# Optimization experiments

Measured on AMD Instinct MI355X. Metric: run time of the kernel, lower is better.

## Reference

```python
import jax, jax.numpy as jnp
import numpy as np

N_NODES = 100000
N_EDGES = 1600000
IN, HID, OUT = 128, 128, 64


def setup_inputs() -> dict:
    key = jax.random.key(0)
    ks = jax.random.split(key, 12)
    x = jax.random.normal(ks[0], (N_NODES, IN), dtype=jnp.float32)
    src = jax.random.randint(ks[1], (N_EDGES,), 0, N_NODES, dtype=jnp.int32)
    dst = jax.random.randint(ks[2], (N_EDGES,), 0, N_NODES, dtype=jnp.int32)

    def lin(k, fan_in, fan_out):
        return jax.random.normal(k, (fan_in, fan_out), dtype=jnp.float32) / jnp.sqrt(jnp.float32(fan_in))

    return {
        "x": x, "src": src, "dst": dst,
        "w_self_0": lin(ks[3], IN, HID), "w_neigh_0": lin(ks[4], IN, HID), "b_0": jnp.zeros((HID,), jnp.float32),
        "w_self_1": lin(ks[5], HID, HID), "w_neigh_1": lin(ks[6], HID, HID), "b_1": jnp.zeros((HID,), jnp.float32),
        "w_self_2": lin(ks[7], HID, OUT), "w_neigh_2": lin(ks[8], HID, OUT), "b_2": jnp.zeros((OUT,), jnp.float32),
    }


def reference(x, src, dst, w_self_0, w_neigh_0, b_0, w_self_1, w_neigh_1, b_1, w_self_2, w_neigh_2, b_2):
    n = x.shape[0]
    # in-degree per dst node; zero-degree nodes keep aggregated 0 (clamp avoids div-by-0)
    deg = jax.ops.segment_sum(jnp.ones_like(dst, dtype=x.dtype), dst, num_segments=n)
    inv_deg = (1.0 / jnp.maximum(deg, 1.0))[:, None]

    def sage_layer(h, w_s, w_n, b):
        # irregular gather of src features, segment-mean over dst
        agg = jax.ops.segment_sum(h[src], dst, num_segments=n) * inv_deg
        return h @ w_s + agg @ w_n + b

    h = jax.nn.relu(sage_layer(x, w_self_0, w_neigh_0, b_0))   # dropout = identity (eval)
    h = jax.nn.relu(sage_layer(h, w_self_1, w_neigh_1, b_1))
    return sage_layer(h, w_self_2, w_neigh_2, b_2)
```

## Files before the change

kernel.cpp:

```cpp
#include <hip/hip_runtime.h>


#define NN 100000
#define NE 1600000
#define BSH 7
#define BND 128
#define NB  782
#define NBLKS 512
#define EPB ((NE + NBLKS - 1) / NBLKS)
#define STOT (NB * NBLKS)
#define SCAN_E 2048
#define NSB ((STOT + SCAN_E - 1) / SCAN_E)
#define GEMM_BLOCKS 1563

typedef __attribute__((ext_vector_type(8))) short short8;
typedef __attribute__((ext_vector_type(4))) float f32x4;
typedef unsigned int uint;
typedef unsigned short ushort;

__device__ inline ushort f2bf(float f) {
    uint u = __float_as_uint(f);
    u += 0x7FFFu + ((u >> 16) & 1u);
    return (ushort)(u >> 16);
}
__device__ inline float bf_lo(uint w) { return __uint_as_float(w << 16); }
__device__ inline float bf_hi(uint w) { return __uint_as_float(w & 0xFFFF0000u); }

template<int NCS, int NCN, bool XF32, bool ABF, bool WLDS>
__device__ void gemm_body(int wid, int tid, int nthr,
    const void* __restrict__ Hv, const ushort* __restrict__ Wf,
    const float* __restrict__ bias, void* __restrict__ Av, ushort* __restrict__ Bt)
{
    constexpr int NCT = (NCS + NCN) / 16;
    const short8* wp;
    if constexpr (WLDS) {
        __shared__ short8 wl[NCT * 4 * 64];
        uint4* dl = (uint4*)wl;
        const uint4* sg = (const uint4*)Wf;
        for (int i = tid; i < NCT * 4 * 64; i += nthr) dl[i] = sg[i];
        __syncthreads();
        wp = wl;
    } else {
        wp = (const short8*)Wf;
    }
    if (wid >= NN / 16) return;
    const int lane = tid & 63;
    const int m = lane & 15;
    const int q = lane >> 4;

    short8 af[4];
    if (XF32) {
        const float* hp = (const float*)Hv + (size_t)(wid * 16 + m) * 128;
        #pragma unroll
        for (int kt = 0; kt < 4; ++kt) {
            const float4 f0 = *(const float4*)(hp + kt * 32 + q * 8);
            const float4 f1 = *(const float4*)(hp + kt * 32 + q * 8 + 4);
            short8 v;
            v[0] = (short)f2bf(f0.x); v[1] = (short)f2bf(f0.y);
            v[2] = (short)f2bf(f0.z); v[3] = (short)f2bf(f0.w);
            v[4] = (short)f2bf(f1.x); v[5] = (short)f2bf(f1.y);
            v[6] = (short)f2bf(f1.z); v[7] = (short)f2bf(f1.w);
            af[kt] = v;
        }
    } else {
        const short8* hp = (const short8*)((const ushort*)Hv + (size_t)(wid * 16 + m) * 128);
        #pragma unroll
        for (int kt = 0; kt < 4; ++kt) af[kt] = hp[kt * 4 + q];
    }

    f32x4 acc[NCT];
    #pragma unroll
    for (int i = 0; i < NCT; ++i) acc[i] = (f32x4){0.f, 0.f, 0.f, 0.f};

    #pragma unroll
    for (int ct = 0; ct < NCT; ++ct) {
        #pragma unroll
        for (int kt = 0; kt < 4; ++kt) {
            const short8 bf = wp[(ct * 4 + kt) * 64 + lane];
            acc[ct] = __builtin_amdgcn_mfma_f32_16x16x32_bf16(af[kt], bf, acc[ct], 0, 0, 0);
        }
    }

    const int r0 = wid * 16 + q * 4;
    #pragma unroll
    for (int ct = 0; ct < NCS / 16; ++ct) {
        const int c = ct * 16 + m;
        const float bv = bias[c];
        #pragma unroll
        for (int r = 0; r < 4; ++r) {
            const float v = acc[ct][r] + bv;
            if (ABF) ((ushort*)Av)[(size_t)(r0 + r) * NCS + c] = f2bf(v);
            else     ((float*) Av)[(size_t)(r0 + r) * NCS + c] = v;
        }
    }
    #pragma unroll
    for (int ct = NCS / 16; ct < NCT; ++ct) {
        const int c = ct * 16 + m - NCS;
        #pragma unroll
        for (int r = 0; r < 4; ++r)
            Bt[(size_t)(r0 + r) * NCN + c] = f2bf(acc[ct][r]);
    }
}

template<int NCS, int NCN, bool XF32, bool ABF>
__global__ __launch_bounds__(512) void gemm_mfma_k(
    const void* __restrict__ Hv, const ushort* __restrict__ Wf,
    const float* __restrict__ bias, void* __restrict__ Av, ushort* __restrict__ Bt)
{
    gemm_body<NCS, NCN, XF32, ABF, true>(
        (blockIdx.x * 512 + threadIdx.x) >> 6, threadIdx.x, 512, Hv, Wf, bias, Av, Bt);
}

__global__ __launch_bounds__(256) void phist_pack_k(
    const int* __restrict__ dst, int* __restrict__ histG,
    const float* __restrict__ ws0, const float* __restrict__ wn0, ushort* __restrict__ wf0,
    const float* __restrict__ ws1, const float* __restrict__ wn1, ushort* __restrict__ wf1,
    const float* __restrict__ ws2, const float* __restrict__ wn2, ushort* __restrict__ wf2)
{
    __shared__ int h[NB];
    const int t = threadIdx.x;
    if (blockIdx.x < NBLKS) {
        for (int i = t; i < NB; i += 256) h[i] = 0;
        __syncthreads();
        const int blk = blockIdx.x;
        const int e0 = blk * EPB;
        const int e1 = min(e0 + EPB, NE);
        for (int e = e0 + t; e < e1; e += 256)
            atomicAdd(&h[dst[e] >> BSH], 1);
        __syncthreads();
        for (int i = t; i < NB; i += 256)
            histG[i * NBLKS + blk] = h[i];
        return;
    }
    const int b = blockIdx.x - NBLKS;
    const float *ws, *wn; ushort* wf; int ncs, idx;
    if (b < 16)      { ws = ws0; wn = wn0; wf = wf0; ncs = 128; idx = b * 256 + t; }
    else if (b < 32) { ws = ws1; wn = wn1; wf = wf1; ncs = 128; idx = (b - 16) * 256 + t; }
    else             { ws = ws2; wn = wn2; wf = wf2; ncs = 64;  idx = (b - 32) * 256 + t; }
    const int total = (2 * ncs / 16) * 4 * 64;
    if (idx >= total) return;
    const int l = idx & 63;
    const int f = idx >> 6;
    const int kt = f & 3;
    const int ct = f >> 2;
    const int n = ct * 16 + (l & 15);
    const int k0 = kt * 32 + (l >> 4) * 8;
    uint w[4];
    #pragma unroll
    for (int p = 0; p < 4; ++p) {
        const int k = k0 + p * 2;
        float v0, v1;
        if (n < ncs) { v0 = ws[k * ncs + n];         v1 = ws[(k + 1) * ncs + n]; }
        else         { v0 = wn[k * ncs + (n - ncs)]; v1 = wn[(k + 1) * ncs + (n - ncs)]; }
        w[p] = (uint)f2bf(v0) | ((uint)f2bf(v1) << 16);
    }
    uint4 o; o.x = w[0]; o.y = w[1]; o.z = w[2]; o.w = w[3];
    ((uint4*)wf)[idx] = o;
}

__global__ __launch_bounds__(256) void scan1_k(int* __restrict__ data, int* __restrict__ blksum) {
    __shared__ int lds[256];
    const int t = threadIdx.x;
    const int base = blockIdx.x * SCAN_E + t * 8;
    int v[8];
    int s = 0;
    #pragma unroll
    for (int i = 0; i < 8; ++i) {
        const int idx = base + i;
        v[i] = (idx < STOT) ? data[idx] : 0;
        s += v[i];
    }
    lds[t] = s;
    __syncthreads();
    #pragma unroll
    for (int off = 1; off < 256; off <<= 1) {
        const int cur = lds[t];
        const int y = (t >= off) ? lds[t - off] : 0;
        __syncthreads();
        lds[t] = cur + y;
        __syncthreads();
    }
    const int incl = lds[t];
    if (t == 255) blksum[blockIdx.x] = incl;
    int run = incl - s;
    #pragma unroll
    for (int i = 0; i < 8; ++i) {
        const int idx = base + i;
        if (idx < STOT) data[idx] = run;
        run += v[i];
    }
}

__global__ __launch_bounds__(256) void scan3_k(int* __restrict__ data, const int* __restrict__ blksum) {
    __shared__ int lds[256];
    const int t = threadIdx.x;
    lds[t] = (t < NSB) ? blksum[t] : 0;
    __syncthreads();
    #pragma unroll
    for (int off = 1; off < 256; off <<= 1) {
        const int cur = lds[t];
        const int y = (t >= off) ? lds[t - off] : 0;
        __syncthreads();
        lds[t] = cur + y;
        __syncthreads();
    }
    const int add = (blockIdx.x == 0) ? 0 : lds[blockIdx.x - 1];
    const int base = blockIdx.x * SCAN_E + t * 8;
    #pragma unroll
    for (int i = 0; i < 8; ++i) {
        const int idx = base + i;
        if (idx < STOT) data[idx] += add;
    }
}

__global__ __launch_bounds__(256) void pscatter_gemm0_k(
    const int* __restrict__ src, const int* __restrict__ dst,
    const int* __restrict__ histG, int* __restrict__ pb,
    const float* __restrict__ x, const ushort* __restrict__ wf0,
    const float* __restrict__ b0, ushort* __restrict__ Abf, ushort* __restrict__ Bt)
{
    __shared__ int wc[NB];
    const int t = threadIdx.x;
    if (blockIdx.x < NBLKS) {
        const int blk = blockIdx.x;
        for (int i = t; i < NB; i += 256) wc[i] = histG[i * NBLKS + blk];
        __syncthreads();
        const int e0 = blk * EPB;
        const int e1 = min(e0 + EPB, NE);
        for (int e = e0 + t; e < e1; e += 256) {
            const int d = dst[e];
            const int pos = atomicAdd(&wc[d >> BSH], 1);
            pb[pos] = (src[e] << BSH) | (d & (BND - 1));
        }
        return;
    }
    gemm_body<128, 128, true, true, false>(
        ((blockIdx.x - NBLKS) * 256 + t) >> 6, t, 256, x, wf0, b0, Abf, Bt);
}

__global__ __launch_bounds__(256) void bucket_place_k(const int* __restrict__ histG,
                                                      const int* __restrict__ pb,
                                                      int* __restrict__ row,
                                                      int* __restrict__ esrc) {
    __shared__ int cnt[BND], wc[BND], excl[BND], scan[BND];
    const int b = blockIdx.x;
    const int t = threadIdx.x;
    if (t < BND) { cnt[t] = 0; wc[t] = 0; }
    __syncthreads();
    const int s0 = histG[b * NBLKS];
    const int s1 = (b + 1 < NB) ? histG[(b + 1) * NBLKS] : NE;
    for (int e = s0 + t; e < s1; e += 256)
        atomicAdd(&cnt[pb[e] & (BND - 1)], 1);
    __syncthreads();
    if (t < BND) scan[t] = cnt[t];
    __syncthreads();
    for (int off = 1; off < BND; off <<= 1) {
        int nv = 0;
        if (t < BND) {
            nv = scan[t];
            if (t >= off) nv += scan[t - off];
        }
        __syncthreads();
        if (t < BND) scan[t] = nv;
        __syncthreads();
    }
    if (t < BND) {
        const int ex = scan[t] - cnt[t];
        excl[t] = ex;
        const int node = b * BND + t;
        if (node <= NN) row[node] = s0 + ex;
    }
    __syncthreads();
    for (int e = s0 + t; e < s1; e += 256) {
        const int p = pb[e];
        const int dl = p & (BND - 1);
        const int pos = s0 + excl[dl] + atomicAdd(&wc[dl], 1);
        esrc[pos] = p >> BSH;
    }
}

__global__ __launch_bounds__(256) void agg128_k(
    const int* __restrict__ row, const int* __restrict__ esrc,
    const ushort* __restrict__ Bt, const ushort* __restrict__ Abf, ushort* __restrict__ Hb)
{
    const int node = (blockIdx.x * 256 + threadIdx.x) >> 4;
    const int ln = threadIdx.x & 15;
    if (node >= NN) return;
    const int e0 = row[node];
    const int e1 = row[node + 1];
    const uint4* B = (const uint4*)Bt;
    float a0 = 0.f, a1 = 0.f, a2 = 0.f, a3 = 0.f;
    float a4 = 0.f, a5 = 0.f, a6 = 0.f, a7 = 0.f;
    int e = e0;
    for (; e + 8 <= e1; e += 8) {
        int s[8];
        #pragma unroll
        for (int j = 0; j < 8; ++j) s[j] = esrc[e + j];
        uint4 v[8];
        #pragma unroll
        for (int j = 0; j < 8; ++j) v[j] = B[(size_t)s[j] * 16 + ln];
        #pragma unroll
        for (int j = 0; j < 8; ++j) {
            a0 += bf_lo(v[j].x); a1 += bf_hi(v[j].x);
            a2 += bf_lo(v[j].y); a3 += bf_hi(v[j].y);
            a4 += bf_lo(v[j].z); a5 += bf_hi(v[j].z);
            a6 += bf_lo(v[j].w); a7 += bf_hi(v[j].w);
        }
    }
    if (e + 4 <= e1) {
        int s[4];
        #pragma unroll
        for (int j = 0; j < 4; ++j) s[j] = esrc[e + j];
        uint4 v[4];
        #pragma unroll
        for (int j = 0; j < 4; ++j) v[j] = B[(size_t)s[j] * 16 + ln];
        #pragma unroll
        for (int j = 0; j < 4; ++j) {
            a0 += bf_lo(v[j].x); a1 += bf_hi(v[j].x);
            a2 += bf_lo(v[j].y); a3 += bf_hi(v[j].y);
            a4 += bf_lo(v[j].z); a5 += bf_hi(v[j].z);
            a6 += bf_lo(v[j].w); a7 += bf_hi(v[j].w);
        }
        e += 4;
    }
    for (; e < e1; ++e) {
        const uint4 v = B[(size_t)esrc[e] * 16 + ln];
        a0 += bf_lo(v.x); a1 += bf_hi(v.x);
        a2 += bf_lo(v.y); a3 += bf_hi(v.y);
        a4 += bf_lo(v.z); a5 += bf_hi(v.z);
        a6 += bf_lo(v.w); a7 += bf_hi(v.w);
    }
    const int deg = e1 - e0;
    const float invd = (deg > 0) ? 1.0f / (float)deg : 0.0f;
    const uint4 aw = ((const uint4*)Abf)[(size_t)node * 16 + ln];
    const float v0 = fmaxf(bf_lo(aw.x) + a0 * invd, 0.f);
    const float v1 = fmaxf(bf_hi(aw.x) + a1 * invd, 0.f);
    const float v2 = fmaxf(bf_lo(aw.y) + a2 * invd, 0.f);
    const float v3 = fmaxf(bf_hi(aw.y) + a3 * invd, 0.f);
    const float v4 = fmaxf(bf_lo(aw.z) + a4 * invd, 0.f);
    const float v5 = fmaxf(bf_hi(aw.z) + a5 * invd, 0.f);
    const float v6 = fmaxf(bf_lo(aw.w) + a6 * invd, 0.f);
    const float v7 = fmaxf(bf_hi(aw.w) + a7 * invd, 0.f);
    uint4 o;
    o.x = (uint)f2bf(v0) | ((uint)f2bf(v1) << 16);
    o.y = (uint)f2bf(v2) | ((uint)f2bf(v3) << 16);
    o.z = (uint)f2bf(v4) | ((uint)f2bf(v5) << 16);
    o.w = (uint)f2bf(v6) | ((uint)f2bf(v7) << 16);
    ((uint4*)Hb)[(size_t)node * 16 + ln] = o;
}

__global__ __launch_bounds__(256) void agg64_k(
    const int* __restrict__ row, const int* __restrict__ esrc,
    const ushort* __restrict__ Bt, float* __restrict__ out)
{
    const int node = (blockIdx.x * 256 + threadIdx.x) >> 3;
    const int ln = threadIdx.x & 7;
    if (node >= NN) return;
    const int e0 = row[node];
    const int e1 = row[node + 1];
    const uint4* B = (const uint4*)Bt;
    float a0 = 0.f, a1 = 0.f, a2 = 0.f, a3 = 0.f;
    float a4 = 0.f, a5 = 0.f, a6 = 0.f, a7 = 0.f;
    int e = e0;
    for (; e + 8 <= e1; e += 8) {
        int s[8];
        #pragma unroll
        for (int j = 0; j < 8; ++j) s[j] = esrc[e + j];
        uint4 v[8];
        #pragma unroll
        for (int j = 0; j < 8; ++j) v[j] = B[(size_t)s[j] * 8 + ln];
        #pragma unroll
        for (int j = 0; j < 8; ++j) {
            a0 += bf_lo(v[j].x); a1 += bf_hi(v[j].x);
            a2 += bf_lo(v[j].y); a3 += bf_hi(v[j].y);
            a4 += bf_lo(v[j].z); a5 += bf_hi(v[j].z);
            a6 += bf_lo(v[j].w); a7 += bf_hi(v[j].w);
        }
    }
    if (e + 4 <= e1) {
        int s[4];
        #pragma unroll
        for (int j = 0; j < 4; ++j) s[j] = esrc[e + j];
        uint4 v[4];
        #pragma unroll
        for (int j = 0; j < 4; ++j) v[j] = B[(size_t)s[j] * 8 + ln];
        #pragma unroll
        for (int j = 0; j < 4; ++j) {
            a0 += bf_lo(v[j].x); a1 += bf_hi(v[j].x);
            a2 += bf_lo(v[j].y); a3 += bf_hi(v[j].y);
            a4 += bf_lo(v[j].z); a5 += bf_hi(v[j].z);
            a6 += bf_lo(v[j].w); a7 += bf_hi(v[j].w);
        }
        e += 4;
    }
    for (; e < e1; ++e) {
        const uint4 v = B[(size_t)esrc[e] * 8 + ln];
        a0 += bf_lo(v.x); a1 += bf_hi(v.x);
        a2 += bf_lo(v.y); a3 += bf_hi(v.y);
        a4 += bf_lo(v.z); a5 += bf_hi(v.z);
        a6 += bf_lo(v.w); a7 += bf_hi(v.w);
    }
    const int deg = e1 - e0;
    const float invd = (deg > 0) ? 1.0f / (float)deg : 0.0f;
    float4* op = (float4*)(out + (size_t)node * 64 + ln * 8);
    float4 o0 = op[0], o1 = op[1];
    o0.x += a0 * invd; o0.y += a1 * invd;
    o0.z += a2 * invd; o0.w += a3 * invd;
    o1.x += a4 * invd; o1.y += a5 * invd;
    o1.z += a6 * invd; o1.w += a7 * invd;
    op[0] = o0; op[1] = o1;
}

__device__ inline float4 relu4f(float4 v) {
    v.x = fmaxf(v.x, 0.f); v.y = fmaxf(v.y, 0.f);
    v.z = fmaxf(v.z, 0.f); v.w = fmaxf(v.w, 0.f);
    return v;
}
template<int NCOL, bool RELU_IN, bool BIAS>
__global__ __launch_bounds__(256) void gemm_k(
    const float* in, const float* __restrict__ W,
    const float* __restrict__ bias, float* out)
{
    constexpr int K = 128;
    constexpr int QUADS = NCOL / 4;
    constexpr int G = 256 / QUADS;
    constexpr int RPT = 32 / G;
    __shared__ float Wlds[K * NCOL];
    {
        const float4* Wg = reinterpret_cast<const float4*>(W);
        float4* Wl = reinterpret_cast<float4*>(Wlds);
        #pragma unroll
        for (int i = 0; i < K * NCOL / 4 / 256; ++i)
            Wl[threadIdx.x + i * 256] = Wg[threadIdx.x + i * 256];
    }
    __syncthreads();
    const int tx = threadIdx.x % QUADS;
    const int ty = threadIdx.x / QUADS;
    const int row0 = blockIdx.x * 32;
    const float* rp[RPT];
    #pragma unroll
    for (int i = 0; i < RPT; ++i) rp[i] = in + (size_t)(row0 + ty + i * G) * K;
    float acc[RPT][4];
    #pragma unroll
    for (int i = 0; i < RPT; ++i) acc[i][0] = acc[i][1] = acc[i][2] = acc[i][3] = 0.f;
    #pragma unroll 2
    for (int kc = 0; kc < K; kc += 4) {
        float4 h4[RPT];
        #pragma unroll
        for (int i = 0; i < RPT; ++i) {
            h4[i] = *reinterpret_cast<const float4*>(rp[i] + kc);
            if (RELU_IN) h4[i] = relu4f(h4[i]);
        }
        #pragma unroll
        for (int kk = 0; kk < 4; ++kk) {
            const float4 w4 = *reinterpret_cast<const float4*>(&Wlds[(kc + kk) * NCOL + tx * 4]);
            #pragma unroll
            for (int i = 0; i < RPT; ++i) {
                const float hv = (&h4[i].x)[kk];
                acc[i][0] = fmaf(hv, w4.x, acc[i][0]);
                acc[i][1] = fmaf(hv, w4.y, acc[i][1]);
                acc[i][2] = fmaf(hv, w4.z, acc[i][2]);
                acc[i][3] = fmaf(hv, w4.w, acc[i][3]);
            }
        }
    }
    float4 b4 = make_float4(0.f, 0.f, 0.f, 0.f);
    if (BIAS) b4 = *reinterpret_cast<const float4*>(&bias[tx * 4]);
    #pragma unroll
    for (int i = 0; i < RPT; ++i) {
        const int r = row0 + ty + i * G;
        float4 o;
        o.x = acc[i][0] + b4.x; o.y = acc[i][1] + b4.y;
        o.z = acc[i][2] + b4.z; o.w = acc[i][3] + b4.w;
        *reinterpret_cast<float4*>(&out[(size_t)r * NCOL + tx * 4]) = o;
    }
}
__global__ void deg_k(const int* __restrict__ dst, float* __restrict__ deg, int E) {
    const int i = blockIdx.x * blockDim.x + threadIdx.x;
    if (i < E) atomicAdd(&deg[dst[i]], 1.0f);
}
__global__ void inv_k(float* deg, int n) {
    const int i = blockIdx.x * blockDim.x + threadIdx.x;
    if (i < n) deg[i] = 1.0f / fmaxf(deg[i], 1.0f);
}
__global__ __launch_bounds__(256) void scatter128_k(
    const int* __restrict__ src, const int* __restrict__ dst,
    const float* __restrict__ inv, const float* __restrict__ B, float* A, int E) {
    const int lane = threadIdx.x & 63;
    int w = (blockIdx.x * 256 + threadIdx.x) >> 6;
    const int nw = (gridDim.x * 256) >> 6;
    for (int e = w; e < E; e += nw) {
        const int s = src[e], d = dst[e];
        const float sc = inv[d];
        const float2 v = *reinterpret_cast<const float2*>(&B[(size_t)s * 128 + lane * 2]);
        atomicAdd(&A[(size_t)d * 128 + lane * 2    ], v.x * sc);
        atomicAdd(&A[(size_t)d * 128 + lane * 2 + 1], v.y * sc);
    }
}
__global__ __launch_bounds__(256) void scatter64_k(
    const int* __restrict__ src, const int* __restrict__ dst,
    const float* __restrict__ inv, const float* __restrict__ B, float* A, int E) {
    const int lane = threadIdx.x & 63;
    int w = (blockIdx.x * 256 + threadIdx.x) >> 6;
    const int nw = (gridDim.x * 256) >> 6;
    for (int e = w; e < E; e += nw) {
        const int s = src[e], d = dst[e];
        atomicAdd(&A[(size_t)d * 64 + lane], B[(size_t)s * 64 + lane] * inv[d]);
    }
}

extern "C" void kernel_launch(void* const* d_in, const int* in_sizes, int n_in,
                              void* d_out, int out_size, void* d_ws, size_t ws_size,
                              hipStream_t stream) {
    const float* x   = (const float*)d_in[0];
    const int*   src = (const int*)  d_in[1];
    const int*   dst = (const int*)  d_in[2];
    const float* ws0 = (const float*)d_in[3];
    const float* wn0 = (const float*)d_in[4];
    const float* b0  = (const float*)d_in[5];
    const float* ws1 = (const float*)d_in[6];
    const float* wn1 = (const float*)d_in[7];
    const float* b1  = (const float*)d_in[8];
    const float* ws2 = (const float*)d_in[9];
    const float* wn2 = (const float*)d_in[10];
    const float* b2  = (const float*)d_in[11];
    float* out = (float*)d_out;

    const size_t O_BLK  = 4096;
    const size_t O_ROW  = 16384;
    const size_t O_WF0  = 417792;
    const size_t O_WF1  = 483328;
    const size_t O_WF2  = 548864;
    const size_t O_ESRC = 581632;
    const size_t O_PB   = 6983680;
    const size_t O_A    = 14286848;
    const size_t O_BT   = 39890944;
    const size_t O_HB   = 65495040;
    const size_t NEED   = 91095040;

    if (ws_size >= NEED) {
        int*    blks  = (int*)   ((char*)d_ws + O_BLK);
        int*    row   = (int*)   ((char*)d_ws + O_ROW);
        ushort* wf0   = (ushort*)((char*)d_ws + O_WF0);
        ushort* wf1   = (ushort*)((char*)d_ws + O_WF1);
        ushort* wf2   = (ushort*)((char*)d_ws + O_WF2);
        int*    esrc  = (int*)   ((char*)d_ws + O_ESRC);
        int*    pb    = (int*)   ((char*)d_ws + O_PB);
        ushort* Abf   = (ushort*)((char*)d_ws + O_A);
        ushort* Bt    = (ushort*)((char*)d_ws + O_BT);
        ushort* Hb    = (ushort*)((char*)d_ws + O_HB);
        int*    histG = (int*)   ((char*)d_ws + O_HB);

        phist_pack_k<<<NBLKS + 40, 256, 0, stream>>>(dst, histG,
            ws0, wn0, wf0, ws1, wn1, wf1, ws2, wn2, wf2);
        scan1_k<<<NSB, 256, 0, stream>>>(histG, blks);
        scan3_k<<<NSB, 256, 0, stream>>>(histG, blks);
        pscatter_gemm0_k<<<NBLKS + GEMM_BLOCKS, 256, 0, stream>>>(
            src, dst, histG, pb, x, wf0, b0, Abf, Bt);
        bucket_place_k<<<NB, 256, 0, stream>>>(histG, pb, row, esrc);

        const int AGG128_BLOCKS = (NN + 15) / 16;
        const int AGG64_BLOCKS  = (NN + 31) / 32;
        const int GEMM512_BLOCKS = (NN / 16 + 7) / 8;

        agg128_k<<<AGG128_BLOCKS, 256, 0, stream>>>(row, esrc, Bt, Abf, Hb);
        gemm_mfma_k<128, 128, false, true ><<<GEMM512_BLOCKS, 512, 0, stream>>>(Hb, wf1, b1, Abf, Bt);
        agg128_k<<<AGG128_BLOCKS, 256, 0, stream>>>(row, esrc, Bt, Abf, Hb);
        gemm_mfma_k<64, 64, false, false><<<GEMM512_BLOCKS, 512, 0, stream>>>(Hb, wf2, b2, out, Bt);
        agg64_k<<<AGG64_BLOCKS, 256, 0, stream>>>(row, esrc, Bt, out);
    } else {
        float* inv = (float*)d_ws;
        float* H0  = (float*)((char*)d_ws + (1u << 20));
        float* Bf  = H0 + (size_t)NN * 128;
        const int GB = NN / 32;
        const int SC_BLOCKS = 4096;
        hipMemsetAsync(inv, 0, NN * sizeof(float), stream);
        deg_k<<<(NE + 255) / 256, 256, 0, stream>>>(dst, inv, NE);
        inv_k<<<(NN + 255) / 256, 256, 0, stream>>>(inv, NN);
        gemm_k<128, false, false><<<GB, 256, 0, stream>>>(x, wn0, nullptr, Bf);
        gemm_k<128, false, true ><<<GB, 256, 0, stream>>>(x, ws0, b0, H0);
        scatter128_k<<<SC_BLOCKS, 256, 0, stream>>>(src, dst, inv, Bf, H0, NE);
        gemm_k<128, true, false><<<GB, 256, 0, stream>>>(H0, wn1, nullptr, Bf);
        gemm_k<128, true, true ><<<GB, 256, 0, stream>>>(H0, ws1, b1, H0);
        scatter128_k<<<SC_BLOCKS, 256, 0, stream>>>(src, dst, inv, Bf, H0, NE);
        gemm_k<64, true, false><<<GB, 256, 0, stream>>>(H0, wn2, nullptr, Bf);
        gemm_k<64, true, true ><<<GB, 256, 0, stream>>>(H0, ws2, b2, out);
        scatter64_k<<<SC_BLOCKS, 256, 0, stream>>>(src, dst, inv, Bf, out, NE);
    }
}
```

Before: 376.5 us.

## Stage layer-0 weights in LDS, halve partition blocks, and deepen gather batches

Measured after the change: 370.2 us. No clear change (-1.7%).

```diff
diff --git a/kernel.cpp b/kernel.cpp
--- a/kernel.cpp
+++ b/kernel.cpp
@@ -6,12 +6,12 @@
 #define BSH 7
 #define BND 128
 #define NB  782
-#define NBLKS 512
+#define NBLKS 256
 #define EPB ((NE + NBLKS - 1) / NBLKS)
 #define STOT (NB * NBLKS)
 #define SCAN_E 2048
 #define NSB ((STOT + SCAN_E - 1) / SCAN_E)
-#define GEMM_BLOCKS 1563
+#define GEMM0_BLOCKS 782
 
 typedef __attribute__((ext_vector_type(8))) short short8;
 typedef __attribute__((ext_vector_type(4))) float f32x4;
@@ -26,23 +26,12 @@
 __device__ inline float bf_lo(uint w) { return __uint_as_float(w << 16); }
 __device__ inline float bf_hi(uint w) { return __uint_as_float(w & 0xFFFF0000u); }
 
-template<int NCS, int NCN, bool XF32, bool ABF, bool WLDS>
-__device__ void gemm_body(int wid, int tid, int nthr,
-    const void* __restrict__ Hv, const ushort* __restrict__ Wf,
+template<int NCS, int NCN, bool XF32, bool ABF>
+__device__ void gemm_body(int wid, int tid,
+    const void* __restrict__ Hv, const short8* __restrict__ wp,
     const float* __restrict__ bias, void* __restrict__ Av, ushort* __restrict__ Bt)
 {
     constexpr int NCT = (NCS + NCN) / 16;
-    const short8* wp;
-    if constexpr (WLDS) {
-        __shared__ short8 wl[NCT * 4 * 64];
-        uint4* dl = (uint4*)wl;
-        const uint4* sg = (const uint4*)Wf;
-        for (int i = tid; i < NCT * 4 * 64; i += nthr) dl[i] = sg[i];
-        __syncthreads();
-        wp = wl;
-    } else {
-        wp = (const short8*)Wf;
-    }
     if (wid >= NN / 16) return;
     const int lane = tid & 63;
     const int m = lane & 15;
@@ -107,8 +96,14 @@
     const void* __restrict__ Hv, const ushort* __restrict__ Wf,
     const float* __restrict__ bias, void* __restrict__ Av, ushort* __restrict__ Bt)
 {
-    gemm_body<NCS, NCN, XF32, ABF, true>(
-        (blockIdx.x * 512 + threadIdx.x) >> 6, threadIdx.x, 512, Hv, Wf, bias, Av, Bt);
+    constexpr int NCT = (NCS + NCN) / 16;
+    __shared__ short8 wl[NCT * 4 * 64];
+    uint4* dl = (uint4*)wl;
+    const uint4* sg = (const uint4*)Wf;
+    for (int i = threadIdx.x; i < NCT * 4 * 64; i += 512) dl[i] = sg[i];
+    __syncthreads();
+    gemm_body<NCS, NCN, XF32, ABF>(
+        (blockIdx.x * 512 + threadIdx.x) >> 6, threadIdx.x, Hv, wl, bias, Av, Bt);
 }
 
 __global__ __launch_bounds__(256) void phist_pack_k(
@@ -213,29 +208,33 @@
     }
 }
 
-__global__ __launch_bounds__(256) void pscatter_gemm0_k(
+__global__ __launch_bounds__(512) void pscatter_gemm0_k(
     const int* __restrict__ src, const int* __restrict__ dst,
     const int* __restrict__ histG, int* __restrict__ pb,
     const float* __restrict__ x, const ushort* __restrict__ wf0,
     const float* __restrict__ b0, ushort* __restrict__ Abf, ushort* __restrict__ Bt)
 {
-    __shared__ int wc[NB];
+    __shared__ uint4 sh[4096];
     const int t = threadIdx.x;
     if (blockIdx.x < NBLKS) {
+        int* wc = (int*)sh;
         const int blk = blockIdx.x;
-        for (int i = t; i < NB; i += 256) wc[i] = histG[i * NBLKS + blk];
+        for (int i = t; i < NB; i += 512) wc[i] = histG[i * NBLKS + blk];
         __syncthreads();
         const int e0 = blk * EPB;
         const int e1 = min(e0 + EPB, NE);
-        for (int e = e0 + t; e < e1; e += 256) {
+        for (int e = e0 + t; e < e1; e += 512) {
             const int d = dst[e];
             const int pos = atomicAdd(&wc[d >> BSH], 1);
             pb[pos] = (src[e] << BSH) | (d & (BND - 1));
         }
         return;
     }
-    gemm_body<128, 128, true, true, false>(
-        ((blockIdx.x - NBLKS) * 256 + t) >> 6, t, 256, x, wf0, b0, Abf, Bt);
+    const uint4* sg = (const uint4*)wf0;
+    for (int i = t; i < 4096; i += 512) sh[i] = sg[i];
+    __syncthreads();
+    gemm_body<128, 128, true, true>(
+        ((blockIdx.x - NBLKS) * 512 + t) >> 6, t, x, (const short8*)sh, b0, Abf, Bt);
 }
 
 __global__ __launch_bounds__(256) void bucket_place_k(const int* __restrict__ histG,
@@ -279,6 +278,24 @@
     }
 }
 
+template<int NBAT, int RS>
+__device__ inline void agg_batch(const int* __restrict__ esrc, int e,
+                                 const uint4* __restrict__ B, int ln, float* a) {
+    int s[NBAT];
+    #pragma unroll
+    for (int j = 0; j < NBAT; ++j) s[j] = esrc[e + j];
+    uint4 v[NBAT];
+    #pragma unroll
+    for (int j = 0; j < NBAT; ++j) v[j] = B[(size_t)s[j] * RS + ln];
+    #pragma unroll
+    for (int j = 0; j < NBAT; ++j) {
+        a[0] += bf_lo(v[j].x); a[1] += bf_hi(v[j].x);
+        a[2] += bf_lo(v[j].y); a[3] += bf_hi(v[j].y);
+        a[4] += bf_lo(v[j].z); a[5] += bf_hi(v[j].z);
+        a[6] += bf_lo(v[j].w); a[7] += bf_hi(v[j].w);
+    }
+}
+
 __global__ __launch_bounds__(256) void agg128_k(
     const int* __restrict__ row, const int* __restrict__ esrc,
     const ushort* __restrict__ Bt, const ushort* __restrict__ Abf, ushort* __restrict__ Hb)
@@ -289,58 +306,23 @@
     const int e0 = row[node];
     const int e1 = row[node + 1];
     const uint4* B = (const uint4*)Bt;
-    float a0 = 0.f, a1 = 0.f, a2 = 0.f, a3 = 0.f;
-    float a4 = 0.f, a5 = 0.f, a6 = 0.f, a7 = 0.f;
+    float a[8] = {0.f, 0.f, 0.f, 0.f, 0.f, 0.f, 0.f, 0.f};
     int e = e0;
-    for (; e + 8 <= e1; e += 8) {
-        int s[8];
-        #pragma unroll
-        for (int j = 0; j < 8; ++j) s[j] = esrc[e + j];
-        uint4 v[8];
-        #pragma unroll
-        for (int j = 0; j < 8; ++j) v[j] = B[(size_t)s[j] * 16 + ln];
-        #pragma unroll
-        for (int j = 0; j < 8; ++j) {
-            a0 += bf_lo(v[j].x); a1 += bf_hi(v[j].x);
-            a2 += bf_lo(v[j].y); a3 += bf_hi(v[j].y);
-            a4 += bf_lo(v[j].z); a5 += bf_hi(v[j].z);
-            a6 += bf_lo(v[j].w); a7 += bf_hi(v[j].w);
-        }
-    }
-    if (e + 4 <= e1) {
-        int s[4];
-        #pragma unroll
-        for (int j = 0; j < 4; ++j) s[j] = esrc[e + j];
-        uint4 v[4];
-        #pragma unroll
-        for (int j = 0; j < 4; ++j) v[j] = B[(size_t)s[j] * 16 + ln];
-        #pragma unroll
-        for (int j = 0; j < 4; ++j) {
-            a0 += bf_lo(v[j].x); a1 += bf_hi(v[j].x);
-            a2 += bf_lo(v[j].y); a3 += bf_hi(v[j].y);
-            a4 += bf_lo(v[j].z); a5 += bf_hi(v[j].z);
-            a6 += bf_lo(v[j].w); a7 += bf_hi(v[j].w);
-        }
-        e += 4;
-    }
-    for (; e < e1; ++e) {
-        const uint4 v = B[(size_t)esrc[e] * 16 + ln];
-        a0 += bf_lo(v.x); a1 += bf_hi(v.x);
-        a2 += bf_lo(v.y); a3 += bf_hi(v.y);
-        a4 += bf_lo(v.z); a5 += bf_hi(v.z);
-        a6 += bf_lo(v.w); a7 += bf_hi(v.w);
-    }
+    for (; e + 16 <= e1; e += 16) agg_batch<16, 16>(esrc, e, B, ln, a);
+    if (e + 8 <= e1) { agg_batch<8, 16>(esrc, e, B, ln, a); e += 8; }
+    if (e + 4 <= e1) { agg_batch<4, 16>(esrc, e, B, ln, a); e += 4; }
+    for (; e < e1; ++e) agg_batch<1, 16>(esrc, e, B, ln, a);
     const int deg = e1 - e0;
     const float invd = (deg > 0) ? 1.0f / (float)deg : 0.0f;
     const uint4 aw = ((const uint4*)Abf)[(size_t)node * 16 + ln];
-    const float v0 = fmaxf(bf_lo(aw.x) + a0 * invd, 0.f);
-    const float v1 = fmaxf(bf_hi(aw.x) + a1 * invd, 0.f);
-    const float v2 = fmaxf(bf_lo(aw.y) + a2 * invd, 0.f);
-    const float v3 = fmaxf(bf_hi(aw.y) + a3 * invd, 0.f);
-    const float v4 = fmaxf(bf_lo(aw.z) + a4 * invd, 0.f);
-    const float v5 = fmaxf(bf_hi(aw.z) + a5 * invd, 0.f);
-    const float v6 = fmaxf(bf_lo(aw.w) + a6 * invd, 0.f);
-    const float v7 = fmaxf(bf_hi(aw.w) + a7 * invd, 0.f);
+    const float v0 = fmaxf(bf_lo(aw.x) + a[0] * invd, 0.f);
+    const float v1 = fmaxf(bf_hi(aw.x) + a[1] * invd, 0.f);
+    const float v2 = fmaxf(bf_lo(aw.y) + a[2] * invd, 0.f);
+    const float v3 = fmaxf(bf_hi(aw.y) + a[3] * invd, 0.f);
+    const float v4 = fmaxf(bf_lo(aw.z) + a[4] * invd, 0.f);
+    const float v5 = fmaxf(bf_hi(aw.z) + a[5] * invd, 0.f);
+    const float v6 = fmaxf(bf_lo(aw.w) + a[6] * invd, 0.f);
+    const float v7 = fmaxf(bf_hi(aw.w) + a[7] * invd, 0.f);
     uint4 o;
     o.x = (uint)f2bf(v0) | ((uint)f2bf(v1) << 16);
     o.y = (uint)f2bf(v2) | ((uint)f2bf(v3) << 16);
@@ -359,55 +341,20 @@
     const int e0 = row[node];
     const int e1 = row[node + 1];
     const uint4* B = (const uint4*)Bt;
-    float a0 = 0.f, a1 = 0.f, a2 = 0.f, a3 = 0.f;
-    float a4 = 0.f, a5 = 0.f, a6 = 0.f, a7 = 0.f;
+    float a[8] = {0.f, 0.f, 0.f, 0.f, 0.f, 0.f, 0.f, 0.f};
     int e = e0;
-    for (; e + 8 <= e1; e += 8) {
-        int s[8];
-        #pragma unroll
-        for (int j = 0; j < 8; ++j) s[j] = esrc[e + j];
-        uint4 v[8];
-        #pragma unroll
-        for (int j = 0; j < 8; ++j) v[j] = B[(size_t)s[j] * 8 + ln];
-        #pragma unroll
-        for (int j = 0; j < 8; ++j) {
-            a0 += bf_lo(v[j].x); a1 += bf_hi(v[j].x);
-            a2 += bf_lo(v[j].y); a3 += bf_hi(v[j].y);
-            a4 += bf_lo(v[j].z); a5 += bf_hi(v[j].z);
-            a6 += bf_lo(v[j].w); a7 += bf_hi(v[j].w);
-        }
-    }
-    if (e + 4 <= e1) {
-        int s[4];
-        #pragma unroll
-        for (int j = 0; j < 4; ++j) s[j] = esrc[e + j];
-        uint4 v[4];
-        #pragma unroll
-        for (int j = 0; j < 4; ++j) v[j] = B[(size_t)s[j] * 8 + ln];
-        #pragma unroll
-        for (int j = 0; j < 4; ++j) {
-            a0 += bf_lo(v[j].x); a1 += bf_hi(v[j].x);
-            a2 += bf_lo(v[j].y); a3 += bf_hi(v[j].y);
-            a4 += bf_lo(v[j].z); a5 += bf_hi(v[j].z);
-            a6 += bf_lo(v[j].w); a7 += bf_hi(v[j].w);
-        }
-        e += 4;
-    }
-    for (; e < e1; ++e) {
-        const uint4 v = B[(size_t)esrc[e] * 8 + ln];
-        a0 += bf_lo(v.x); a1 += bf_hi(v.x);
-        a2 += bf_lo(v.y); a3 += bf_hi(v.y);
-        a4 += bf_lo(v.z); a5 += bf_hi(v.z);
-        a6 += bf_lo(v.w); a7 += bf_hi(v.w);
-    }
+    for (; e + 16 <= e1; e += 16) agg_batch<16, 8>(esrc, e, B, ln, a);
+    if (e + 8 <= e1) { agg_batch<8, 8>(esrc, e, B, ln, a); e += 8; }
+    if (e + 4 <= e1) { agg_batch<4, 8>(esrc, e, B, ln, a); e += 4; }
+    for (; e < e1; ++e) agg_batch<1, 8>(esrc, e, B, ln, a);
     const int deg = e1 - e0;
     const float invd = (deg > 0) ? 1.0f / (float)deg : 0.0f;
     float4* op = (float4*)(out + (size_t)node * 64 + ln * 8);
     float4 o0 = op[0], o1 = op[1];
-    o0.x += a0 * invd; o0.y += a1 * invd;
-    o0.z += a2 * invd; o0.w += a3 * invd;
-    o1.x += a4 * invd; o1.y += a5 * invd;
-    o1.z += a6 * invd; o1.w += a7 * invd;
+    o0.x += a[0] * invd; o0.y += a[1] * invd;
+    o0.z += a[2] * invd; o0.w += a[3] * invd;
+    o1.x += a[4] * invd; o1.y += a[5] * invd;
+    o1.z += a[6] * invd; o1.w += a[7] * invd;
     op[0] = o0; op[1] = o1;
 }
 
@@ -555,7 +502,7 @@
             ws0, wn0, wf0, ws1, wn1, wf1, ws2, wn2, wf2);
         scan1_k<<<NSB, 256, 0, stream>>>(histG, blks);
         scan3_k<<<NSB, 256, 0, stream>>>(histG, blks);
-        pscatter_gemm0_k<<<NBLKS + GEMM_BLOCKS, 256, 0, stream>>>(
+        pscatter_gemm0_k<<<NBLKS + GEMM0_BLOCKS, 512, 0, stream>>>(
             src, dst, histG, pb, x, wf0, b0, Abf, Bt);
         bucket_place_k<<<NB, 256, 0, stream>>>(histG, pb, row, esrc);
 
```
